# Optimization experiments

Hardware: AMD Instinct MI355X
Metric: run time of the kernel (lower is better)

The kernel has to match this reference:

```python
import jax, jax.numpy as jnp
import numpy as np

N = 1_000_000      # rows
D = 64             # input feature dim
INNER = 16         # inner_dim (Cholesky size)
OUT = 64           # out_dim (proj output)
NSEG = 100_000     # num_segments
NET_OUT = INNER * (INNER + 1) // 2 + INNER  # 152


def setup_inputs() -> dict:
    key = jax.random.key(0)
    k0, k1, k2, k3 = jax.random.split(key, 4)
    data = jax.random.normal(k0, (N, D), dtype=jnp.float32)
    segments = jax.random.randint(k1, (N,), 0, NSEG)
    # LazyInMLP([]) -> single Dense(net_out_dim) with kernel_init=normal(stddev=1e-2)
    W = jax.random.normal(k2, (D, NET_OUT), dtype=jnp.float32) * 0.01
    b = jnp.zeros((NET_OUT,), dtype=jnp.float32)
    # proj Dense(out_dim, use_bias=False), lecun-normal-ish scale
    proj_W = jax.random.normal(k3, (INNER, OUT), dtype=jnp.float32) * (1.0 / np.sqrt(INNER))
    return {"data": data, "segments": segments, "num_segments": NSEG,
            "W": W, "b": b, "proj_W": proj_W}


def reference(data, segments, num_segments, W, b, proj_W):
    # MLP (zero hidden layers -> single Dense)
    net_out = data @ W + b                      # [N, 152]
    t = net_out[:, :INNER]                      # [N, 16]
    y = net_out[:, INNER:]                      # [N, 136]

    # vectorized un_chol: fill lower triangle with tanh, then softplus the diag
    rows, cols = jnp.tril_indices(INNER)
    L = jnp.zeros((data.shape[0], INNER, INNER), dtype=data.dtype)
    L = L.at[:, rows, cols].set(jnp.tanh(y))
    di = jnp.arange(INNER)
    L = L.at[:, di, di].set(jax.nn.softplus(L[:, di, di]))
    F = jnp.einsum('nik,njk->nij', L, L)        # L @ L.T, [N, 16, 16]

    # segment reductions (reduction='sum')
    F_red = jax.ops.segment_sum(F, segments, num_segments=num_segments)  # [S,16,16]
    t_red = jax.ops.segment_sum(t, segments, num_segments=num_segments)  # [S,16]

    F_masked = F_red + jnp.eye(INNER, dtype=F_red.dtype)
    F_inv = jnp.linalg.inv(F_masked)            # batched small-matrix inverse
    # NOTE: faithful to source einsum '...ij,...j->...j' (sums over i, keeps j)
    theta = jnp.einsum('sij,sj->sj', F_inv, t_red)  # [S, 16]

    # inner_dim != out_dim -> proj Dense (no bias)
    return theta @ proj_W                       # [S, 64]
```

## Files before the change

kernel.cpp:

```cpp
#include <hip/hip_runtime.h>
#include <hip/hip_bf16.h>


#define N_PTS   1000000
#define DIM     64
#define INNER   16
#define OUTD    64
#define NSEG    100000
#define NTRI    136
#define NET_OUT 152
#define NB      391
#define SEGW    7
#define NWAVES  ((NSEG + SEGW - 1) / SEGW)
#define MAINB   ((NWAVES + 3) / 4)

typedef short bf16x8 __attribute__((ext_vector_type(8)));
typedef float f32x4  __attribute__((ext_vector_type(4)));

__device__ __host__ __forceinline__ constexpr int tri(int i) { return i * (i + 1) / 2; }

__device__ __forceinline__ float fast_tanh(float x) {
    float e = __expf(2.0f * x);
    return 1.0f - __fdividef(2.0f, e + 1.0f);
}
__device__ __forceinline__ float fast_softplus(float x) {
    return __logf(1.0f + __expf(x));
}
__device__ __forceinline__ short f2bf(float f) {
    unsigned u = __float_as_uint(f);
    return (short)((u + 0x7FFF + ((u >> 16) & 1)) >> 16);
}

__device__ __forceinline__ void wave_lds_sync() {
    __builtin_amdgcn_wave_barrier();
    __builtin_amdgcn_s_waitcnt(0xC07F);
    __builtin_amdgcn_wave_barrier();
}

__device__ __forceinline__ void ecoord(int e, int& r, int& c, bool& dg) {
    int rr = 0;
    #pragma unroll
    for (int k = 1; k < 16; ++k) rr = (e >= tri(k)) ? k : rr;
    r = rr; c = e - tri(rr); dg = (c == rr);
}

__global__ __launch_bounds__(256) void hist_kernel(const int* __restrict__ segs,
                                                   int* __restrict__ cnt,
                                                   int* __restrict__ rank)
{
    int t = blockIdx.x * 256 + threadIdx.x;
    if (t < N_PTS) rank[t] = atomicAdd(&cnt[segs[t]], 1);
}

__global__ __launch_bounds__(256) void scan_blocks(const int* __restrict__ cnt,
                                                   int* __restrict__ off,
                                                   int* __restrict__ bsum)
{
    __shared__ int sh[256];
    const int t = threadIdx.x;
    const int i = blockIdx.x * 256 + t;
    int v = (i < NSEG) ? cnt[i] : 0;
    sh[t] = v;
    __syncthreads();
    #pragma unroll
    for (int d = 1; d < 256; d <<= 1) {
        int add = (t >= d) ? sh[t - d] : 0;
        __syncthreads();
        sh[t] += add;
        __syncthreads();
    }
    if (i < NSEG) off[i] = sh[t] - v;
    if (t == 255) bsum[blockIdx.x] = sh[t];
}

__global__ __launch_bounds__(512) void scan_top(int* __restrict__ bsum)
{
    __shared__ int sh[512];
    const int t = threadIdx.x;
    int v = (t < NB) ? bsum[t] : 0;
    sh[t] = v;
    __syncthreads();
    #pragma unroll
    for (int d = 1; d < 512; d <<= 1) {
        int add = (t >= d) ? sh[t - d] : 0;
        __syncthreads();
        sh[t] += add;
        __syncthreads();
    }
    if (t < NB) bsum[t] = sh[t] - v;
}

__global__ __launch_bounds__(256) void scan_add(int* __restrict__ off,
                                                const int* __restrict__ bsum)
{
    int i = blockIdx.x * 256 + threadIdx.x;
    if (i < NSEG) off[i] += bsum[blockIdx.x];
}

__global__ __launch_bounds__(256) void scatter_kernel(const int* __restrict__ segs,
                                                      const int* __restrict__ off,
                                                      const int* __restrict__ rank,
                                                      int* __restrict__ sorted)
{
    int t = blockIdx.x * 256 + threadIdx.x;
    if (t < N_PTS) sorted[off[segs[t]] + rank[t]] = t;
}

__global__ __launch_bounds__(256, 2)
void main_kernel(const float* __restrict__ data,
                 const int*   __restrict__ segs,
                 const int*   __restrict__ sorted,
                 const int*   __restrict__ off,
                 const int*   __restrict__ cnt,
                 const float* __restrict__ W,
                 const float* __restrict__ bias,
                 float* __restrict__ Fred,
                 float* __restrict__ tred)
{
    __shared__ __align__(16) unsigned short lds[4 * 6144];
    const int l = threadIdx.x & 63;
    const int w = threadIdx.x >> 6;
    unsigned short* Lw = &lds[w * 6144];
    const int c = l & 15;
    const int q = l >> 4;

    #pragma unroll
    for (int u = 0; u < 48; ++u) ((unsigned*)Lw)[u * 64 + l] = 0u;
    wave_lds_sync();

    bf16x8 wf[10][2];
    float  bT[10];
    #pragma unroll
    for (int T = 0; T < 10; ++T) {
        #pragma unroll
        for (int ks = 0; ks < 2; ++ks) {
            bf16x8 f;
            #pragma unroll
            for (int j = 0; j < 8; ++j) {
                int k = 32 * ks + 8 * q + j;
                int n = 16 * T + c;
                f[j] = (n < NET_OUT) ? f2bf(W[k * NET_OUT + n]) : (short)0;
            }
            wf[T][ks] = f;
        }
        int n = 16 * T + c;
        bT[T] = (n < NET_OUT) ? bias[n] : 0.0f;
    }

    int  rcoff[9];
    bool dgm[9];
    #pragma unroll
    for (int T = 1; T <= 9; ++T) {
        int e = 16 * (T - 1) + c;
        int re, ce; bool dg;
        ecoord(e, re, ce, dg);
        rcoff[T - 1] = re * 24 + ce;
        dgm[T - 1]   = dg;
    }
    const bool v9 = (c < 8);

    int trim[4], mrow[4];
    #pragma unroll
    for (int r = 0; r < 4; ++r) { mrow[r] = 4 * q + r; trim[r] = tri(4 * q + r); }

    const int wave_id = blockIdx.x * 4 + w;
    const int ws0 = wave_id * SEGW;
    if (ws0 >= NSEG) return;
    const int ws1 = min(ws0 + SEGW, NSEG);
    int g = off[ws0];
    const int gend = off[ws1 - 1] + cnt[ws1 - 1];

    f32x4 facc = {0.f, 0.f, 0.f, 0.f};
    float tcarry = 0.f;
    int a_start = 0;

    while (g < gend) {
        const int nv = min(16, gend - g);
        const int idx  = g + min(c, nv - 1);
        const int p    = sorted[idx];
        const int pn   = sorted[min(idx + 1, N_PTS - 1)];
        const int ssp  = segs[p];
        const int sspn = segs[pn];
        const bool flag = (idx == N_PTS - 1) || (sspn != ssp);
        const unsigned long long bm = __ballot(l < 16 && c < nv && flag);

        bf16x8 af[2];
        #pragma unroll
        for (int ks = 0; ks < 2; ++ks) {
            const float4* dp = (const float4*)(data + (size_t)p * DIM + 32 * ks + 8 * q);
            float4 x0 = dp[0], x1 = dp[1];
            bf16x8 f;
            f[0] = f2bf(x0.x); f[1] = f2bf(x0.y); f[2] = f2bf(x0.z); f[3] = f2bf(x0.w);
            f[4] = f2bf(x1.x); f[5] = f2bf(x1.y); f[6] = f2bf(x1.z); f[7] = f2bf(x1.w);
            af[ks] = f;
        }
        f32x4 acc[10];
        #pragma unroll
        for (int T = 0; T < 10; ++T) {
            f32x4 z = {0.f, 0.f, 0.f, 0.f};
            z = __builtin_amdgcn_mfma_f32_16x16x32_bf16(af[0], wf[T][0], z, 0, 0, 0);
            acc[T] = __builtin_amdgcn_mfma_f32_16x16x32_bf16(af[1], wf[T][1], z, 0, 0, 0);
        }

        float s0 = acc[0][0] + bT[0];
        float s1 = s0 + acc[0][1] + bT[0];
        float s2 = s1 + acc[0][2] + bT[0];
        float s3 = s2 + acc[0][3] + bT[0];
        float u  = s3;
        float v16 = __shfl_up(u, 16, 64);
        float v32 = __shfl_up(u, 32, 64);
        float v48 = __shfl_up(u, 48, 64);
        float excl = (q >= 1 ? v16 : 0.f) + (q >= 2 ? v32 : 0.f) + (q >= 3 ? v48 : 0.f);
        float P0 = excl + s0, P1 = excl + s1, P2 = excl + s2, P3 = excl + s3;

        wave_lds_sync();
        #pragma unroll
        for (int T = 1; T <= 9; ++T) {
            #pragma unroll
            for (int r = 0; r < 4; ++r) {
                float v = fast_tanh(acc[T][r] + bT[T]);
                if (dgm[T - 1]) v = fast_softplus(v);
                if (T < 9 || v9)
                    Lw[mrow[r] * 384 + rcoff[T - 1]] = (unsigned short)f2bf(v);
            }
        }
        wave_lds_sync();

        for (int i = 0; i < nv; ++i) {
            bf16x8 lf = {0, 0, 0, 0, 0, 0, 0, 0};
            if (q < 2)
                lf = *(const bf16x8*)(Lw + i * 384 + c * 24 + q * 8);
            facc = __builtin_amdgcn_mfma_f32_16x16x32_bf16(lf, lf, facc, 0, 0, 0);

            if ((bm >> i) & 1) {
                const int sid = __shfl(ssp, i, 64);
                int rs = i & 3;
                float vi = (rs == 0) ? P0 : (rs == 1) ? P1 : (rs == 2) ? P2 : P3;
                float Pi = __shfl(vi, ((i >> 2) << 4) | c, 64);
                float Pe = 0.f;
                if (a_start > 0) {
                    int aa = a_start - 1, ra = aa & 3;
                    float va = (ra == 0) ? P0 : (ra == 1) ? P1 : (ra == 2) ? P2 : P3;
                    Pe = __shfl(va, ((aa >> 2) << 4) | c, 64);
                }
                float ts = Pi - Pe + tcarry;
                if (l < 16) tred[(size_t)sid * INNER + c] = ts;
                tcarry = 0.f;
                #pragma unroll
                for (int r = 0; r < 4; ++r)
                    if (c <= mrow[r])
                        Fred[(size_t)sid * NTRI + trim[r] + c] = facc[r];
                facc = (f32x4){0.f, 0.f, 0.f, 0.f};
                a_start = i + 1;
            }
        }
        if (a_start < nv) {
            int ii = nv - 1, rs = ii & 3;
            float vi = (rs == 0) ? P0 : (rs == 1) ? P1 : (rs == 2) ? P2 : P3;
            float Pi = __shfl(vi, ((ii >> 2) << 4) | c, 64);
            float Pe = 0.f;
            if (a_start > 0) {
                int aa = a_start - 1, ra = aa & 3;
                float va = (ra == 0) ? P0 : (ra == 1) ? P1 : (ra == 2) ? P2 : P3;
                Pe = __shfl(va, ((aa >> 2) << 4) | c, 64);
            }
            tcarry += Pi - Pe;
        }
        a_start = 0;
        g += nv;
    }
}

__global__ __launch_bounds__(256, 2)
void seg_kernel(const float* __restrict__ Fred,
                const float* __restrict__ tred,
                const int*   __restrict__ cnt,
                const float* __restrict__ projW,
                float* __restrict__ out)
{
    const int s = blockIdx.x * 256 + threadIdx.x;
    if (s >= NSEG) return;
    float* orow = out + (size_t)s * OUTD;

    if (cnt[s] == 0) {
        float4 zz = {0.f, 0.f, 0.f, 0.f};
        #pragma unroll
        for (int oc = 0; oc < OUTD; oc += 4) *(float4*)(orow + oc) = zz;
        return;
    }

    float a[NTRI];
    const float4* f4 = (const float4*)(Fred + (size_t)s * NTRI);
    #pragma unroll
    for (int qq = 0; qq < NTRI / 4; ++qq) {
        float4 v = f4[qq];
        a[4 * qq + 0] = v.x; a[4 * qq + 1] = v.y;
        a[4 * qq + 2] = v.z; a[4 * qq + 3] = v.w;
    }
    #pragma unroll
    for (int ii = 0; ii < INNER; ++ii) a[tri(ii) + ii] += 1.0f;

    #pragma unroll
    for (int j = 0; j < INNER; ++j) {
        float d = a[tri(j) + j];
        #pragma unroll
        for (int k = 0; k < j; ++k)
            d = fmaf(-a[tri(j) + k], a[tri(j) + k], d);
        d = sqrtf(d);
        a[tri(j) + j] = d;
        float dinv = __fdividef(1.0f, d);
        #pragma unroll
        for (int ii = j + 1; ii < INNER; ++ii) {
            float v = a[tri(ii) + j];
            #pragma unroll
            for (int k = 0; k < j; ++k)
                v = fmaf(-a[tri(ii) + k], a[tri(j) + k], v);
            a[tri(ii) + j] = v * dinv;
        }
    }
    float z[INNER];
    #pragma unroll
    for (int ii = 0; ii < INNER; ++ii) {
        float v = 1.0f;
        #pragma unroll
        for (int k = 0; k < ii; ++k)
            v = fmaf(-a[tri(ii) + k], z[k], v);
        z[ii] = __fdividef(v, a[tri(ii) + ii]);
    }
    float x[INNER];
    #pragma unroll
    for (int ii = INNER - 1; ii >= 0; --ii) {
        float v = z[ii];
        #pragma unroll
        for (int k = ii + 1; k < INNER; ++k)
            v = fmaf(-a[tri(k) + ii], x[k], v);
        x[ii] = __fdividef(v, a[tri(ii) + ii]);
    }
    float theta[INNER];
    const float4* t4 = (const float4*)(tred + (size_t)s * INNER);
    #pragma unroll
    for (int qq = 0; qq < 4; ++qq) {
        float4 v = t4[qq];
        theta[4 * qq + 0] = v.x * x[4 * qq + 0];
        theta[4 * qq + 1] = v.y * x[4 * qq + 1];
        theta[4 * qq + 2] = v.z * x[4 * qq + 2];
        theta[4 * qq + 3] = v.w * x[4 * qq + 3];
    }
    for (int oc = 0; oc < OUTD; oc += 8) {
        float acc[8] = {0, 0, 0, 0, 0, 0, 0, 0};
        #pragma unroll
        for (int j = 0; j < INNER; ++j) {
            float th = theta[j];
            #pragma unroll
            for (int uu = 0; uu < 8; ++uu)
                acc[uu] = fmaf(th, projW[j * OUTD + oc + uu], acc[uu]);
        }
        float4 v0 = {acc[0], acc[1], acc[2], acc[3]};
        float4 v1 = {acc[4], acc[5], acc[6], acc[7]};
        ((float4*)(orow + oc))[0] = v0;
        ((float4*)(orow + oc))[1] = v1;
    }
}

extern "C" void kernel_launch(void* const* d_in, const int* in_sizes, int n_in,
                              void* d_out, int out_size, void* d_ws, size_t ws_size,
                              hipStream_t stream)
{
    const float* data  = (const float*)d_in[0];
    const int*   segs  = (const int*)d_in[1];
    const float* W     = (const float*)d_in[3];
    const float* bias  = (const float*)d_in[4];
    const float* projW = (const float*)d_in[5];

    int* cnt     = (int*)d_ws;
    int* off     = cnt + NSEG;
    int* bsum    = off + NSEG;
    int* rank    = bsum + 512;
    int* sorted  = rank + N_PTS;
    float* Fred  = (float*)(sorted + N_PTS);
    float* tred  = Fred + (size_t)NSEG * NTRI;

    hipMemsetAsync(cnt, 0, NSEG * sizeof(int), stream);

    hist_kernel   <<<(N_PTS + 255) / 256, 256, 0, stream>>>(segs, cnt, rank);
    scan_blocks   <<<NB, 256, 0, stream>>>(cnt, off, bsum);
    scan_top      <<<1, 512, 0, stream>>>(bsum);
    scan_add      <<<NB, 256, 0, stream>>>(off, bsum);
    scatter_kernel<<<(N_PTS + 255) / 256, 256, 0, stream>>>(segs, off, rank, sorted);
    main_kernel   <<<MAINB, 256, 0, stream>>>(data, segs, sorted, off, cnt, W, bias, Fred, tred);
    seg_kernel    <<<NB, 256, 0, stream>>>(Fred, tred, cnt, projW, (float*)d_out);
}
```

Before: 715.6 us.

## Pack two rows per MFMA, derive segment ids from offsets, prefetch sorted indices

The main kernel now computes segment membership from the per-wave segment end offsets held in registers. This replaces the dependent segs[] gathers that were used to find segment boundaries. The L tile layout in LDS is compacted from a 24-stride to a 16-stride layout, so one 32-wide MFMA can accumulate two rows' L·Lᵀ at once when no segment boundary falls between them. The next chunk's sorted index is prefetched a loop iteration ahead, and the smaller LDS footprint lets launch bounds rise to 3 blocks per CU. This adds branchy pair logic, with extra split MFMAs at segment boundaries, and raises register pressure.

Result: slower. 1.005 ms (+40.5%).

```diff
diff --git a/kernel.cpp b/kernel.cpp
--- a/kernel.cpp
+++ b/kernel.cpp
@@ -106,9 +106,8 @@
     if (t < N_PTS) sorted[off[segs[t]] + rank[t]] = t;
 }
 
-__global__ __launch_bounds__(256, 2)
+__global__ __launch_bounds__(256, 3)
 void main_kernel(const float* __restrict__ data,
-                 const int*   __restrict__ segs,
                  const int*   __restrict__ sorted,
                  const int*   __restrict__ off,
                  const int*   __restrict__ cnt,
@@ -117,15 +116,31 @@
                  float* __restrict__ Fred,
                  float* __restrict__ tred)
 {
-    __shared__ __align__(16) unsigned short lds[4 * 6144];
+    __shared__ __align__(16) unsigned short lds[4 * 4096];
     const int l = threadIdx.x & 63;
     const int w = threadIdx.x >> 6;
-    unsigned short* Lw = &lds[w * 6144];
+    unsigned short* Lw = &lds[w * 4096];
     const int c = l & 15;
     const int q = l >> 4;
 
-    #pragma unroll
-    for (int u = 0; u < 48; ++u) ((unsigned*)Lw)[u * 64 + l] = 0u;
+    const int wave_id = blockIdx.x * 4 + w;
+    const int ws0 = wave_id * SEGW;
+    if (ws0 >= NSEG) return;
+    const int ws1 = min(ws0 + SEGW, NSEG);
+
+    int Ek[SEGW];
+    int gend = 0;
+    #pragma unroll
+    for (int k = 0; k < SEGW; ++k) {
+        const int s = ws0 + k;
+        if (s < ws1) { gend = off[s] + cnt[s]; Ek[k] = gend; }
+        else           Ek[k] = 0x7fffffff;
+    }
+    int g = off[ws0];
+    if (g >= gend) return;
+
+    #pragma unroll
+    for (int u = 0; u < 32; ++u) ((unsigned*)Lw)[u * 64 + l] = 0u;
     wave_lds_sync();
 
     bf16x8 wf[10][2];
@@ -154,7 +169,7 @@
         int e = 16 * (T - 1) + c;
         int re, ce; bool dg;
         ecoord(e, re, ce, dg);
-        rcoff[T - 1] = re * 24 + ce;
+        rcoff[T - 1] = re * 16 + ce;
         dgm[T - 1]   = dg;
     }
     const bool v9 = (c < 8);
@@ -162,26 +177,30 @@
     int trim[4], mrow[4];
     #pragma unroll
     for (int r = 0; r < 4; ++r) { mrow[r] = 4 * q + r; trim[r] = tri(4 * q + r); }
-
-    const int wave_id = blockIdx.x * 4 + w;
-    const int ws0 = wave_id * SEGW;
-    if (ws0 >= NSEG) return;
-    const int ws1 = min(ws0 + SEGW, NSEG);
-    int g = off[ws0];
-    const int gend = off[ws1 - 1] + cnt[ws1 - 1];
 
     f32x4 facc = {0.f, 0.f, 0.f, 0.f};
     float tcarry = 0.f;
     int a_start = 0;
 
+    const int lofs = c * 16 + (q & 1) * 8 + (q >> 1) * 256;
+
+    int idx = min(g + c, gend - 1);
+    int p   = sorted[idx];
+
     while (g < gend) {
-        const int nv = min(16, gend - g);
-        const int idx  = g + min(c, nv - 1);
-        const int p    = sorted[idx];
-        const int pn   = sorted[min(idx + 1, N_PTS - 1)];
-        const int ssp  = segs[p];
-        const int sspn = segs[pn];
-        const bool flag = (idx == N_PTS - 1) || (sspn != ssp);
+        const int nv   = min(16, gend - g);
+        const int gn   = g + nv;
+        const int idxn = min(gn + c, gend - 1);
+        const int pnx  = sorted[idxn];
+
+        int segl = 0;
+        bool flag = false;
+        #pragma unroll
+        for (int k = 0; k < SEGW; ++k) {
+            segl += (idx >= Ek[k]) ? 1 : 0;
+            flag |= (idx == Ek[k] - 1);
+        }
+        const int sidv = ws0 + segl;
         const unsigned long long bm = __ballot(l < 16 && c < nv && flag);
 
         bf16x8 af[2];
@@ -221,53 +240,69 @@
                 float v = fast_tanh(acc[T][r] + bT[T]);
                 if (dgm[T - 1]) v = fast_softplus(v);
                 if (T < 9 || v9)
-                    Lw[mrow[r] * 384 + rcoff[T - 1]] = (unsigned short)f2bf(v);
+                    Lw[mrow[r] * 256 + rcoff[T - 1]] = (unsigned short)f2bf(v);
             }
         }
         wave_lds_sync();
 
-        for (int i = 0; i < nv; ++i) {
-            bf16x8 lf = {0, 0, 0, 0, 0, 0, 0, 0};
-            if (q < 2)
-                lf = *(const bf16x8*)(Lw + i * 384 + c * 24 + q * 8);
-            facc = __builtin_amdgcn_mfma_f32_16x16x32_bf16(lf, lf, facc, 0, 0, 0);
-
-            if ((bm >> i) & 1) {
-                const int sid = __shfl(ssp, i, 64);
-                int rs = i & 3;
-                float vi = (rs == 0) ? P0 : (rs == 1) ? P1 : (rs == 2) ? P2 : P3;
-                float Pi = __shfl(vi, ((i >> 2) << 4) | c, 64);
-                float Pe = 0.f;
-                if (a_start > 0) {
-                    int aa = a_start - 1, ra = aa & 3;
-                    float va = (ra == 0) ? P0 : (ra == 1) ? P1 : (ra == 2) ? P2 : P3;
-                    Pe = __shfl(va, ((aa >> 2) << 4) | c, 64);
+        auto flush = [&](int i) {
+            const int sid = __shfl(sidv, i, 64);
+            const int rs = i & 3;
+            float vi = (rs == 0) ? P0 : (rs == 1) ? P1 : (rs == 2) ? P2 : P3;
+            float Pi = __shfl(vi, ((i >> 2) << 4) | c, 64);
+            float Pe = 0.f;
+            if (a_start > 0) {
+                const int aa = a_start - 1, ra = aa & 3;
+                float va = (ra == 0) ? P0 : (ra == 1) ? P1 : (ra == 2) ? P2 : P3;
+                Pe = __shfl(va, ((aa >> 2) << 4) | c, 64);
+            }
+            float ts = Pi - Pe + tcarry;
+            if (l < 16) tred[(size_t)sid * INNER + c] = ts;
+            tcarry = 0.f;
+            #pragma unroll
+            for (int r = 0; r < 4; ++r)
+                if (c <= mrow[r])
+                    Fred[(size_t)sid * NTRI + trim[r] + c] = facc[r];
+            facc = (f32x4){0.f, 0.f, 0.f, 0.f};
+            a_start = i + 1;
+        };
+
+        const int npair = (nv + 1) >> 1;
+        for (int j = 0; j < npair; ++j) {
+            const int i0 = 2 * j, i1 = i0 + 1;
+            bf16x8 lf = *(const bf16x8*)(Lw + i0 * 256 + lofs);
+            const bool vld1 = (i1 < nv);
+            const bool f0 = (bm >> i0) & 1;
+            if (vld1 && !f0) {
+                facc = __builtin_amdgcn_mfma_f32_16x16x32_bf16(lf, lf, facc, 0, 0, 0);
+                if ((bm >> i1) & 1) flush(i1);
+            } else {
+                const bf16x8 zz = {0, 0, 0, 0, 0, 0, 0, 0};
+                bf16x8 lo = (q < 2) ? lf : zz;
+                facc = __builtin_amdgcn_mfma_f32_16x16x32_bf16(lo, lo, facc, 0, 0, 0);
+                if (f0) flush(i0);
+                if (vld1) {
+                    bf16x8 hi = (q >= 2) ? lf : zz;
+                    facc = __builtin_amdgcn_mfma_f32_16x16x32_bf16(hi, hi, facc, 0, 0, 0);
+                    if ((bm >> i1) & 1) flush(i1);
                 }
-                float ts = Pi - Pe + tcarry;
-                if (l < 16) tred[(size_t)sid * INNER + c] = ts;
-                tcarry = 0.f;
-                #pragma unroll
-                for (int r = 0; r < 4; ++r)
-                    if (c <= mrow[r])
-                        Fred[(size_t)sid * NTRI + trim[r] + c] = facc[r];
-                facc = (f32x4){0.f, 0.f, 0.f, 0.f};
-                a_start = i + 1;
             }
         }
+
         if (a_start < nv) {
-            int ii = nv - 1, rs = ii & 3;
+            const int ii = nv - 1, rs = ii & 3;
             float vi = (rs == 0) ? P0 : (rs == 1) ? P1 : (rs == 2) ? P2 : P3;
             float Pi = __shfl(vi, ((ii >> 2) << 4) | c, 64);
             float Pe = 0.f;
             if (a_start > 0) {
-                int aa = a_start - 1, ra = aa & 3;
+                const int aa = a_start - 1, ra = aa & 3;
                 float va = (ra == 0) ? P0 : (ra == 1) ? P1 : (ra == 2) ? P2 : P3;
                 Pe = __shfl(va, ((aa >> 2) << 4) | c, 64);
             }
             tcarry += Pi - Pe;
         }
         a_start = 0;
-        g += nv;
+        g = gn; idx = idxn; p = pnx;
     }
 }
 
@@ -387,6 +422,6 @@
     scan_top      <<<1, 512, 0, stream>>>(bsum);
     scan_add      <<<NB, 256, 0, stream>>>(off, bsum);
     scatter_kernel<<<(N_PTS + 255) / 256, 256, 0, stream>>>(segs, off, rank, sorted);
-    main_kernel   <<<MAINB, 256, 0, stream>>>(data, segs, sorted, off, cnt, W, bias, Fred, tred);
+    main_kernel   <<<MAINB, 256, 0, stream>>>(data, sorted, off, cnt, W, bias, Fred, tred);
     seg_kernel    <<<NB, 256, 0, stream>>>(Fred, tred, cnt, projW, (float*)d_out);
 }
```
